# Optimization experiments

Hardware: AMD Instinct MI355X
Metric: run time of the kernel (lower is better)

The kernel has to match this reference:

```python
import jax, jax.numpy as jnp
import numpy as np

KDIM = 128

def setup_inputs() -> dict:
    key = jax.random.key(0)
    kq, kk, kv = jax.random.split(key, 3)
    B, S, D = 8, 2048, KDIM
    q = jax.random.normal(kq, (B, S, D), dtype=jnp.float32)
    k = jax.random.normal(kk, (B, S, D), dtype=jnp.float32)
    v = jax.random.normal(kv, (B, S, D), dtype=jnp.float32)
    # causal mask: True = masked (future keys)
    mask = jnp.triu(jnp.ones((S, S), dtype=bool), k=1)
    return {"q": q, "k": k, "v": v, "mask": mask}

def reference(q, k, v, mask):
    # scores: [B, S_q, S_k]
    scores = jnp.einsum("bqd,bkd->bqk", q, k) / jnp.sqrt(jnp.asarray(KDIM, q.dtype))
    scores = jnp.where(mask, -jnp.inf, scores)
    attn = jax.nn.softmax(scores, axis=-1)
    return jnp.einsum("bqk,bkd->bqd", attn, v)
```

## Files before the change

### kernel.cpp

```cpp
#include <hip/hip_runtime.h>
#include <hip/hip_bf16.h>

#define S_LEN 2048
#define DHEAD 128

typedef __bf16 bf16x8 __attribute__((ext_vector_type(8)));
typedef float  f32x16 __attribute__((ext_vector_type(16)));

union PK { __bf16 h[2]; unsigned u; };
union BW { unsigned w4[4]; bf16x8 v; };
union FU { float f; unsigned u; };

__device__ __forceinline__ bf16x8 cvt8(float4 a, float4 b) {
  bf16x8 r;
  r[0] = (__bf16)a.x; r[1] = (__bf16)a.y; r[2] = (__bf16)a.z; r[3] = (__bf16)a.w;
  r[4] = (__bf16)b.x; r[5] = (__bf16)b.y; r[6] = (__bf16)b.z; r[7] = (__bf16)b.w;
  return r;
}

#if __has_builtin(__builtin_amdgcn_permlane32_swap)
__device__ __forceinline__ void plswap(unsigned &a, unsigned &b) {
  auto r = __builtin_amdgcn_permlane32_swap((int)a, (int)b, false, false);
  a = (unsigned)r[0];
  b = (unsigned)r[1];
}
#else
__device__ __forceinline__ void plswap(unsigned &a, unsigned &b) {
  const bool hi = (threadIdx.x & 32) != 0;
  const unsigned ea = (unsigned)__shfl_xor((int)a, 32);
  const unsigned eb = (unsigned)__shfl_xor((int)b, 32);
  const unsigned na = hi ? eb : a;
  const unsigned nb = hi ? b : ea;
  a = na; b = nb;
}
#endif
__device__ __forceinline__ float xmax32(float x) {
  FU a, b; a.f = x; b.f = x; plswap(a.u, b.u); return fmaxf(a.f, b.f);
}
__device__ __forceinline__ float xsum32(float x) {
  FU a, b; a.f = x; b.f = x; plswap(a.u, b.u); return a.f + b.f;
}

__global__ __launch_bounds__(256) void kvprep(const float* __restrict__ K,
                                              const float* __restrict__ V,
                                              char* __restrict__ Kp,
                                              char* __restrict__ Vp, int nkb) {
  __shared__ float t[32 * 132];
  const int tid = threadIdx.x;
  if ((int)blockIdx.x < nkb) {
    const int bid = blockIdx.x;
    const int b = bid >> 6, tt = bid & 63;
    const int row = tid >> 3, c8 = tid & 7;
    const float4* src = (const float4*)(K + ((size_t)(b * S_LEN + 32 * tt + row) * DHEAD + 16 * c8));
    float4 f0 = src[0], f1 = src[1], f2 = src[2], f3 = src[3];
    char* dst = Kp + (size_t)(b * 64 + tt) * 8192 + c8 * 1024 + row * 16;
    *(bf16x8*)(dst)       = cvt8(f0, f1);
    *(bf16x8*)(dst + 512) = cvt8(f2, f3);
  } else {
    const int bid = blockIdx.x - nkb;
    const int b = bid >> 6, u = bid & 63;
    const int row = tid >> 3, c8 = tid & 7;
    const float4* src = (const float4*)(V + ((size_t)(b * S_LEN + 32 * u + row) * DHEAD + 16 * c8));
    float4 f0 = src[0], f1 = src[1], f2 = src[2], f3 = src[3];
    float* d = t + row * 132 + 16 * c8;
    *(float4*)(d) = f0; *(float4*)(d + 4) = f1;
    *(float4*)(d + 8) = f2; *(float4*)(d + 12) = f3;
    __syncthreads();
#pragma unroll
    for (int k = 0; k < 2; ++k) {
      const int id = tid * 2 + k;
      const int lq = id & 31, hh = (id >> 5) & 1, s = (id >> 6) & 1, db = (id >> 7) & 3;
      bf16x8 o;
#pragma unroll
      for (int j = 0; j < 8; ++j) o[j] = (__bf16)t[(16 * s + 8 * hh + j) * 132 + 32 * db + lq];
      *(bf16x8*)(Vp + (size_t)(b * 64 + u) * 8192 + id * 16) = o;
    }
  }
}

__global__ __launch_bounds__(256, 2) void attn_fwd(
    const float* __restrict__ Q, const char* __restrict__ Kp,
    const char* __restrict__ Vp, float* __restrict__ Out) {
  __shared__ __align__(16) char lds[38016];

  const int tid  = threadIdx.x;
  const int w    = tid >> 6;
  const int lane = tid & 63;
  const int h    = lane >> 5;
  const int lq   = lane & 31;

  const int bi    = blockIdx.x;
  const int batch = bi & 7;
  const int T     = (bi < 256) ? (63 - (bi >> 3)) : ((bi - 256) >> 3);
  const int q0    = T << 5;

  const float* Qb = Q + (size_t)batch * S_LEN * DHEAD;
  const char*  Kb = Kp + (size_t)batch * (S_LEN * 256) + h * 512 + lq * 16;
  const char*  Vb = Vp + (size_t)batch * (S_LEN * 256) + h * 512 + lq * 16;

  float  mrun = -INFINITY, lrun = 0.f;
  f32x16 ob[4];
#pragma unroll
  for (int db = 0; db < 4; ++db)
#pragma unroll
    for (int r = 0; r < 16; ++r) ob[db][r] = 0.f;

  if (w <= T) {
    bf16x8 kfA[8], kfB[8];

#pragma unroll
    for (int c = 0; c < 8; ++c) kfA[c] = *(const bf16x8*)(Kb + w * 8192 + c * 1024);

    const float scale = 0.12751777903743892f;
    bf16x8 qf[8];
    {
      const float* qp = Qb + (size_t)(q0 + lq) * DHEAD + 8 * h;
#pragma unroll
      for (int ks = 0; ks < 8; ++ks) {
        float4 a = *(const float4*)(qp + 16 * ks);
        float4 b = *(const float4*)(qp + 16 * ks + 4);
        a.x *= scale; a.y *= scale; a.z *= scale; a.w *= scale;
        b.x *= scale; b.y *= scale; b.z *= scale; b.w *= scale;
        qf[ks] = cvt8(a, b);
      }
    }

    auto window = [&](bf16x8 (&kcur)[8], bf16x8 (&knxt)[8], int u) {
      bf16x8 vf[8];
      const char* vb = Vb + u * 8192;
#pragma unroll
      for (int c = 0; c < 8; ++c) vf[c] = *(const bf16x8*)(vb + c * 1024);
      const int tn = (u + 4 <= T) ? (u + 4) : T;
#pragma unroll
      for (int c = 0; c < 8; ++c) knxt[c] = *(const bf16x8*)(Kb + tn * 8192 + c * 1024);
      __builtin_amdgcn_sched_barrier(0);

      f32x16 sa, sb;
#pragma unroll
      for (int r = 0; r < 16; ++r) { sa[r] = 0.f; sb[r] = 0.f; }
      __builtin_amdgcn_s_setprio(1);
#pragma unroll
      for (int ks = 0; ks < 4; ++ks)
        sa = __builtin_amdgcn_mfma_f32_32x32x16_bf16(kcur[ks], qf[ks], sa, 0, 0, 0);
#pragma unroll
      for (int ks = 4; ks < 8; ++ks)
        sb = __builtin_amdgcn_mfma_f32_32x32x16_bf16(kcur[ks], qf[ks], sb, 0, 0, 0);
      __builtin_amdgcn_s_setprio(0);

      float sv[16];
#pragma unroll
      for (int r = 0; r < 16; ++r) sv[r] = sa[r] + sb[r];
      if (u == T) {
#pragma unroll
        for (int r = 0; r < 16; ++r) {
          const int kvr = (r & 3) + 8 * (r >> 2) + 4 * h;
          if (kvr > lq) sv[r] = -INFINITY;
        }
      }

      float m8[8];
#pragma unroll
      for (int r = 0; r < 8; ++r) m8[r] = fmaxf(sv[r], sv[r + 8]);
#pragma unroll
      for (int r = 0; r < 4; ++r) m8[r] = fmaxf(m8[r], m8[r + 4]);
      float mx = fmaxf(fmaxf(m8[0], m8[1]), fmaxf(m8[2], m8[3]));
      mx = xmax32(mx);

      if (__any(mx > mrun + 12.f)) {
        const float mnew = fmaxf(mrun, mx);
        const float al = exp2f(mrun - mnew);
        lrun *= al;
#pragma unroll
        for (int db = 0; db < 4; ++db)
#pragma unroll
          for (int r = 0; r < 16; ++r) ob[db][r] *= al;
        mrun = mnew;
      }

      float pv[16];
#pragma unroll
      for (int r = 0; r < 16; ++r) pv[r] = exp2f(sv[r] - mrun);
      float s8[8];
#pragma unroll
      for (int r = 0; r < 8; ++r) s8[r] = pv[r] + pv[r + 8];
#pragma unroll
      for (int r = 0; r < 4; ++r) s8[r] = s8[r] + s8[r + 4];
      lrun += xsum32((s8[0] + s8[1]) + (s8[2] + s8[3]));

      unsigned cc[8];
#pragma unroll
      for (int i = 0; i < 8; ++i) {
        PK pk;
        pk.h[0] = (__bf16)pv[2 * i];
        pk.h[1] = (__bf16)pv[2 * i + 1];
        cc[i] = pk.u;
      }
      plswap(cc[0], cc[2]); plswap(cc[1], cc[3]);
      plswap(cc[4], cc[6]); plswap(cc[5], cc[7]);
      BW pb0, pb1;
      pb0.w4[0] = cc[0]; pb0.w4[1] = cc[1]; pb0.w4[2] = cc[2]; pb0.w4[3] = cc[3];
      pb1.w4[0] = cc[4]; pb1.w4[1] = cc[5]; pb1.w4[2] = cc[6]; pb1.w4[3] = cc[7];

      __builtin_amdgcn_s_setprio(1);
#pragma unroll
      for (int db = 0; db < 4; ++db) {
        ob[db] = __builtin_amdgcn_mfma_f32_32x32x16_bf16(vf[2 * db],     pb0.v, ob[db], 0, 0, 0);
        ob[db] = __builtin_amdgcn_mfma_f32_32x32x16_bf16(vf[2 * db + 1], pb1.v, ob[db], 0, 0, 0);
      }
      __builtin_amdgcn_s_setprio(0);
    };

    int u = w;
    while (true) {
      window(kfA, kfB, u);
      if (u + 4 > T) break;
      u += 4;
      window(kfB, kfA, u);
      if (u + 4 > T) break;
      u += 4;
    }
  }

  float2* ml   = (float2*)(lds + 36864);
  float*  Lbuf = (float*)(lds + 37888);
  float*  Ob0  = (float*)(lds);
  float*  Ob1  = (float*)(lds + 16896);

  if (h == 0) ml[w * 32 + lq] = make_float2(mrun, lrun);
  __syncthreads();

  float M = -INFINITY;
#pragma unroll
  for (int ww = 0; ww < 4; ++ww) M = fmaxf(M, ml[ww * 32 + lq].x);
  float L = 0.f;
#pragma unroll
  for (int ww = 0; ww < 4; ++ww) {
    float2 v = ml[ww * 32 + lq];
    L += v.y * exp2f(v.x - M);
  }
  const float fw = exp2f(mrun - M);
  if (w == 0 && h == 0) Lbuf[lq] = 1.f / L;

  float* Ob = (w & 1) ? Ob1 : Ob0;
  if (w < 2) {
#pragma unroll
    for (int db = 0; db < 4; ++db)
#pragma unroll
      for (int rr = 0; rr < 4; ++rr) {
        float4 val = { ob[db][4 * rr + 0] * fw, ob[db][4 * rr + 1] * fw,
                       ob[db][4 * rr + 2] * fw, ob[db][4 * rr + 3] * fw };
        *(float4*)(Ob + lq * 132 + 32 * db + 8 * rr + 4 * h) = val;
      }
  }
  __syncthreads();
  if (w >= 2) {
#pragma unroll
    for (int db = 0; db < 4; ++db)
#pragma unroll
      for (int rr = 0; rr < 4; ++rr) {
        float* p = Ob + lq * 132 + 32 * db + 8 * rr + 4 * h;
        float4 cur = *(float4*)p;
        cur.x += ob[db][4 * rr + 0] * fw;
        cur.y += ob[db][4 * rr + 1] * fw;
        cur.z += ob[db][4 * rr + 2] * fw;
        cur.w += ob[db][4 * rr + 3] * fw;
        *(float4*)p = cur;
      }
  }
  __syncthreads();

  const int row = tid >> 3;
  const int d0  = (tid & 7) * 16;
  const float inv = Lbuf[row];
  float* orow = Out + ((size_t)(batch * S_LEN + q0 + row)) * DHEAD + d0;
#pragma unroll
  for (int j = 0; j < 4; ++j) {
    float4 a = *(float4*)(Ob0 + row * 132 + d0 + 4 * j);
    float4 b = *(float4*)(Ob1 + row * 132 + d0 + 4 * j);
    float4 o = { (a.x + b.x) * inv, (a.y + b.y) * inv,
                 (a.z + b.z) * inv, (a.w + b.w) * inv };
    *(float4*)(orow + 4 * j) = o;
  }
}

extern "C" void kernel_launch(void* const* d_in, const int* in_sizes, int n_in,
                              void* d_out, int out_size, void* d_ws, size_t ws_size,
                              hipStream_t stream) {
  const float* q = (const float*)d_in[0];
  const float* k = (const float*)d_in[1];
  const float* v = (const float*)d_in[2];
  float* out = (float*)d_out;
  const int B = in_sizes[0] / (S_LEN * DHEAD);

  char* kp = (char*)d_ws;
  char* vp = (char*)d_ws + (size_t)B * S_LEN * 256;

  kvprep<<<dim3(B * 128), dim3(256), 0, stream>>>(k, v, kp, vp, B * 64);
  attn_fwd<<<dim3(B * (S_LEN / 32)), dim3(256), 0, stream>>>(q, kp, vp, out);
}
```

Before: 33.13 us.

## Use 512-thread blocks covering 64 query rows with two wave groups

Each block now handles two adjacent 32-row query tiles, with four waves per tile splitting the key range. This halves the grid to 256 blocks and drops the old heavy-first tile ordering, since the block work now comes in paired tiles. The LDS reduction buffers are doubled to hold both groups. exp2f is also replaced by the raw hardware exp2 builtin, which skips denormal and range handling. The risk is a coarser grid and uneven work across the two groups in a block, since the second tile runs one more window.

```diff
diff --git a/kernel.cpp b/kernel.cpp
--- a/kernel.cpp
+++ b/kernel.cpp
@@ -17,6 +17,12 @@
   r[4] = (__bf16)b.x; r[5] = (__bf16)b.y; r[6] = (__bf16)b.z; r[7] = (__bf16)b.w;
   return r;
 }
+
+#if __has_builtin(__builtin_amdgcn_exp2f)
+__device__ __forceinline__ float exp2h(float x) { return __builtin_amdgcn_exp2f(x); }
+#else
+__device__ __forceinline__ float exp2h(float x) { return exp2f(x); }
+#endif
 
 #if __has_builtin(__builtin_amdgcn_permlane32_swap)
 __device__ __forceinline__ void plswap(unsigned &a, unsigned &b) {
@@ -78,21 +84,24 @@
   }
 }
 
-__global__ __launch_bounds__(256, 2) void attn_fwd(
+__global__ __launch_bounds__(512, 2) void attn_fwd(
     const float* __restrict__ Q, const char* __restrict__ Kp,
     const char* __restrict__ Vp, float* __restrict__ Out) {
-  __shared__ __align__(16) char lds[38016];
+  __shared__ __align__(16) char lds[69888];
 
   const int tid  = threadIdx.x;
   const int w    = tid >> 6;
   const int lane = tid & 63;
   const int h    = lane >> 5;
   const int lq   = lane & 31;
+  const int qh   = w >> 2;
+  const int kq   = w & 3;
 
   const int bi    = blockIdx.x;
   const int batch = bi & 7;
-  const int T     = (bi < 256) ? (63 - (bi >> 3)) : ((bi - 256) >> 3);
-  const int q0    = T << 5;
+  const int T     = bi >> 3;
+  const int q0g   = (T << 6) + (qh << 5);
+  const int ul    = 2 * T + qh;
 
   const float* Qb = Q + (size_t)batch * S_LEN * DHEAD;
   const char*  Kb = Kp + (size_t)batch * (S_LEN * 256) + h * 512 + lq * 16;
@@ -105,16 +114,16 @@
 #pragma unroll
     for (int r = 0; r < 16; ++r) ob[db][r] = 0.f;
 
-  if (w <= T) {
+  if (kq <= ul) {
     bf16x8 kfA[8], kfB[8];
 
 #pragma unroll
-    for (int c = 0; c < 8; ++c) kfA[c] = *(const bf16x8*)(Kb + w * 8192 + c * 1024);
+    for (int c = 0; c < 8; ++c) kfA[c] = *(const bf16x8*)(Kb + kq * 8192 + c * 1024);
 
     const float scale = 0.12751777903743892f;
     bf16x8 qf[8];
     {
-      const float* qp = Qb + (size_t)(q0 + lq) * DHEAD + 8 * h;
+      const float* qp = Qb + (size_t)(q0g + lq) * DHEAD + 8 * h;
 #pragma unroll
       for (int ks = 0; ks < 8; ++ks) {
         float4 a = *(const float4*)(qp + 16 * ks);
@@ -130,7 +139,7 @@
       const char* vb = Vb + u * 8192;
 #pragma unroll
       for (int c = 0; c < 8; ++c) vf[c] = *(const bf16x8*)(vb + c * 1024);
-      const int tn = (u + 4 <= T) ? (u + 4) : T;
+      const int tn = (u + 4 <= ul) ? (u + 4) : ul;
 #pragma unroll
       for (int c = 0; c < 8; ++c) knxt[c] = *(const bf16x8*)(Kb + tn * 8192 + c * 1024);
       __builtin_amdgcn_sched_barrier(0);
@@ -150,7 +159,7 @@
       float sv[16];
 #pragma unroll
       for (int r = 0; r < 16; ++r) sv[r] = sa[r] + sb[r];
-      if (u == T) {
+      if (u == ul) {
 #pragma unroll
         for (int r = 0; r < 16; ++r) {
           const int kvr = (r & 3) + 8 * (r >> 2) + 4 * h;
@@ -168,7 +177,7 @@
 
       if (__any(mx > mrun + 12.f)) {
         const float mnew = fmaxf(mrun, mx);
-        const float al = exp2f(mrun - mnew);
+        const float al = exp2h(mrun - mnew);
         lrun *= al;
 #pragma unroll
         for (int db = 0; db < 4; ++db)
@@ -179,7 +188,7 @@
 
       float pv[16];
 #pragma unroll
-      for (int r = 0; r < 16; ++r) pv[r] = exp2f(sv[r] - mrun);
+      for (int r = 0; r < 16; ++r) pv[r] = exp2h(sv[r] - mrun);
       float s8[8];
 #pragma unroll
       for (int r = 0; r < 8; ++r) s8[r] = pv[r] + pv[r + 8];
@@ -210,39 +219,39 @@
       __builtin_amdgcn_s_setprio(0);
     };
 
-    int u = w;
+    int u = kq;
     while (true) {
       window(kfA, kfB, u);
-      if (u + 4 > T) break;
+      if (u + 4 > ul) break;
       u += 4;
       window(kfB, kfA, u);
-      if (u + 4 > T) break;
+      if (u + 4 > ul) break;
       u += 4;
     }
   }
 
-  float2* ml   = (float2*)(lds + 36864);
-  float*  Lbuf = (float*)(lds + 37888);
-  float*  Ob0  = (float*)(lds);
-  float*  Ob1  = (float*)(lds + 16896);
-
+  float2* ml   = (float2*)(lds + 67584);
+  float*  Lbuf = (float*)(lds + 69632);
+  char*   Obase = lds + qh * 33792;
+
+  __syncthreads();
   if (h == 0) ml[w * 32 + lq] = make_float2(mrun, lrun);
   __syncthreads();
 
   float M = -INFINITY;
 #pragma unroll
-  for (int ww = 0; ww < 4; ++ww) M = fmaxf(M, ml[ww * 32 + lq].x);
+  for (int ww = 0; ww < 4; ++ww) M = fmaxf(M, ml[(4 * qh + ww) * 32 + lq].x);
   float L = 0.f;
 #pragma unroll
   for (int ww = 0; ww < 4; ++ww) {
-    float2 v = ml[ww * 32 + lq];
-    L += v.y * exp2f(v.x - M);
-  }
-  const float fw = exp2f(mrun - M);
-  if (w == 0 && h == 0) Lbuf[lq] = 1.f / L;
-
-  float* Ob = (w & 1) ? Ob1 : Ob0;
-  if (w < 2) {
+    float2 v = ml[(4 * qh + ww) * 32 + lq];
+    L += v.y * exp2h(v.x - M);
+  }
+  const float fw = exp2h(mrun - M);
+  if (kq == 0 && h == 0) Lbuf[32 * qh + lq] = 1.f / L;
+
+  float* Ob = (float*)(Obase + (kq & 1) * 16896);
+  if (kq < 2) {
 #pragma unroll
     for (int db = 0; db < 4; ++db)
 #pragma unroll
@@ -253,7 +262,7 @@
       }
   }
   __syncthreads();
-  if (w >= 2) {
+  if (kq >= 2) {
 #pragma unroll
     for (int db = 0; db < 4; ++db)
 #pragma unroll
@@ -270,13 +279,17 @@
   __syncthreads();
 
   const int row = tid >> 3;
+  const int g   = row >> 5;
+  const int lr  = row & 31;
   const int d0  = (tid & 7) * 16;
   const float inv = Lbuf[row];
-  float* orow = Out + ((size_t)(batch * S_LEN + q0 + row)) * DHEAD + d0;
+  const float* O0 = (const float*)(lds + g * 33792);
+  const float* O1 = (const float*)(lds + g * 33792 + 16896);
+  float* orow = Out + ((size_t)(batch * S_LEN + (T << 6) + row)) * DHEAD + d0;
 #pragma unroll
   for (int j = 0; j < 4; ++j) {
-    float4 a = *(float4*)(Ob0 + row * 132 + d0 + 4 * j);
-    float4 b = *(float4*)(Ob1 + row * 132 + d0 + 4 * j);
+    float4 a = *(const float4*)(O0 + lr * 132 + d0 + 4 * j);
+    float4 b = *(const float4*)(O1 + lr * 132 + d0 + 4 * j);
     float4 o = { (a.x + b.x) * inv, (a.y + b.y) * inv,
                  (a.z + b.z) * inv, (a.w + b.w) * inv };
     *(float4*)(orow + 4 * j) = o;
@@ -296,5 +309,5 @@
   char* vp = (char*)d_ws + (size_t)B * S_LEN * 256;
 
   kvprep<<<dim3(B * 128), dim3(256), 0, stream>>>(k, v, kp, vp, B * 64);
-  attn_fwd<<<dim3(B * (S_LEN / 32)), dim3(256), 0, stream>>>(q, kp, vp, out);
-}
+  attn_fwd<<<dim3(B * (S_LEN / 64)), dim3(512), 0, stream>>>(q, kp, vp, out);
+}
```

Measured after the change: 39.54 us. 1.19x slower.
